# Kernel optimization log

Measured on AMD Instinct MI355X. Metric: run time of the kernel, lower is better.

## Reference

```python
import jax, jax.numpy as jnp
import numpy as np

B, D = 32, 2048


def setup_inputs() -> dict:
    key = jax.random.key(0)
    ks = jax.random.split(key, 7)
    # torch init: weights ~ N(0, 0.1^2); biases default Linear uniform(-1/sqrt(D), 1/sqrt(D))
    bound = 1.0 / np.sqrt(D)
    return {
        "x": jax.random.normal(ks[0], (B, D), dtype=jnp.float32),
        "Wq": 0.1 * jax.random.normal(ks[1], (D, D), dtype=jnp.float32),
        "bq": jax.random.uniform(ks[2], (D,), minval=-bound, maxval=bound, dtype=jnp.float32),
        "Wk": 0.1 * jax.random.normal(ks[3], (D, D), dtype=jnp.float32),
        "bk": jax.random.uniform(ks[4], (D,), minval=-bound, maxval=bound, dtype=jnp.float32),
        "Wv": 0.1 * jax.random.normal(ks[5], (D, D), dtype=jnp.float32),
        "bv": jax.random.uniform(ks[6], (D,), minval=-bound, maxval=bound, dtype=jnp.float32),
    }


def reference(x, Wq, bq, Wk, bk, Wv, bv):
    # q,k,v: [B, D] feature-wise projections (torch Linear: x @ W^T + b)
    q = x @ Wq.T + bq
    k = x @ Wk.T + bk
    v = x @ Wv.T + bv
    # rank-1 outer product scores[b,i,j] = q[b,i] * k[b,j]  -> [B, D, D]
    scores = q[:, :, None] * k[:, None, :]
    # softmax over dim=1 (as in the original F.softmax(..., dim=1))
    weights = jax.nn.softmax(scores, axis=1)
    # weighted V sum: out[b,i] = sum_j weights[b,i,j] * v[b,j]  -> [B, D]
    out = jnp.einsum("bij,bj->bi", weights, v)
    return out
```

## Files before the change

kernel.cpp:

```cpp
#include <hip/hip_runtime.h>
#include <math.h>


#define D 2048
#define BATCH 32
#define SEG 132
#define NPART 8

#define PART_STRIDE 196608
#define KDP_OFF 1572864
#define NP_OFF  1708032

#define L2E 1.4426950408889634f

typedef short s16x8 __attribute__((ext_vector_type(8)));
typedef float f32x4 __attribute__((ext_vector_type(4)));

union FragU { s16x8 v; unsigned u[4]; };

__device__ __forceinline__ float fast_exp2(float x) {
#if __has_builtin(__builtin_amdgcn_exp2f)
  return __builtin_amdgcn_exp2f(x);
#else
  return exp2f(x);
#endif
}
__device__ __forceinline__ unsigned pack_rne(float a, float b) {
  unsigned ua = __float_as_uint(a), ub = __float_as_uint(b);
  ua = ua + 0x7FFFu + ((ua >> 16) & 1u);
  ub = ub + 0x7FFFu + ((ub >> 16) & 1u);
  return (ua >> 16) | (ub & 0xFFFF0000u);
}
__device__ __forceinline__ void pack8(const float4& fa, const float4& fb,
                                      FragU& h) {
  h.u[0] = pack_rne(fa.x, fa.y);
  h.u[1] = pack_rne(fa.z, fa.w);
  h.u[2] = pack_rne(fb.x, fb.y);
  h.u[3] = pack_rne(fb.z, fb.w);
}
__device__ __forceinline__ float sum_parts(const float* __restrict__ ws,
                                           size_t o) {
  float s0 = ws[o] + ws[o + PART_STRIDE];
  float s1 = ws[o + 2 * PART_STRIDE] + ws[o + 3 * PART_STRIDE];
  float s2 = ws[o + 4 * PART_STRIDE] + ws[o + 5 * PART_STRIDE];
  float s3 = ws[o + 6 * PART_STRIDE] + ws[o + 7 * PART_STRIDE];
  return (s0 + s1) + (s2 + s3);
}

__global__ __launch_bounds__(256, 4) void k1_proj(
    const float* __restrict__ x, const float* __restrict__ Wq,
    const float* __restrict__ Wk, const float* __restrict__ Wv,
    float* __restrict__ ws) {
  __shared__ float red[4][512];
  const int tid = threadIdx.x;
  const int lane = tid & 63, wv = tid >> 6;
  const int tile = blockIdx.x >> 3, ke = blockIdx.x & 7;
  const int m = tile >> 7, lr = (tile & 127) * 16;
  const float* W = (m == 0) ? Wq : (m == 1) ? Wk : Wv;

  const int kbase = ke * 256 + wv * 64 + (lane >> 4) * 8;
  const float* ap = W + (size_t)(lr + (lane & 15)) * D + kbase;
  const float* xp0 = x + (size_t)(lane & 15) * D + kbase;
  const float* xp1 = xp0 + 16 * D;

  f32x4 acc0 = {0.f, 0.f, 0.f, 0.f}, acc1 = {0.f, 0.f, 0.f, 0.f};
#pragma unroll
  for (int s = 0; s < 2; ++s) {
    const int off = s * 32;
    float4 fa = *(const float4*)(ap + off);
    float4 fb = *(const float4*)(ap + off + 4);
    float4 x0a = *(const float4*)(xp0 + off);
    float4 x0b = *(const float4*)(xp0 + off + 4);
    float4 x1a = *(const float4*)(xp1 + off);
    float4 x1b = *(const float4*)(xp1 + off + 4);
    FragU Ah, Bh0, Bh1;
    pack8(fa, fb, Ah);
    pack8(x0a, x0b, Bh0);
    pack8(x1a, x1b, Bh1);
    acc0 = __builtin_amdgcn_mfma_f32_16x16x32_bf16(Ah.v, Bh0.v, acc0, 0, 0, 0);
    acc1 = __builtin_amdgcn_mfma_f32_16x16x32_bf16(Ah.v, Bh1.v, acc1, 0, 0, 0);
  }
  const int col = lane & 15, rq = (lane >> 4) * 4;
#pragma unroll
  for (int r = 0; r < 4; ++r) {
    red[wv][col * 16 + rq + r] = acc0[r];
    red[wv][(col + 16) * 16 + rq + r] = acc1[r];
  }
  __syncthreads();
  float* part = ws + (size_t)ke * PART_STRIDE + (size_t)m * 65536;
#pragma unroll
  for (int i = tid; i < 512; i += 256) {
    float s = (red[0][i] + red[1][i]) + (red[2][i] + red[3][i]);
    part[(size_t)(i >> 4) * D + lr + (i & 15)] = s;
  }
}

__global__ __launch_bounds__(512, 4) void k3_dz(float* __restrict__ ws,
                                                const float* __restrict__ bq,
                                                const float* __restrict__ bk,
                                                const float* __restrict__ bv) {
  __shared__ float qs[2048];
  __shared__ float zs[512];
  __shared__ float rmx[8], rmn[8];
  __shared__ int cnt[2];
  const int bx = blockIdx.x, t = threadIdx.x;
  const int b = bx >> 4, jc = bx & 15;
  if (t == 0) { cnt[0] = 0; cnt[1] = 0; }

  const size_t qb = (size_t)b * D;
  float4 bb = ((const float4*)bq)[t];
  float4 qv = bb;
#pragma unroll
  for (int p = 0; p < NPART; ++p) {
    float4 pp = ((const float4*)(ws + (size_t)p * PART_STRIDE + qb))[t];
    qv.x += pp.x; qv.y += pp.y; qv.z += pp.z; qv.w += pp.w;
  }
  *(float4*)&qs[t * 4] = qv;
  float mx = fmaxf(fmaxf(qv.x, qv.y), fmaxf(qv.z, qv.w));
  float mn = fminf(fminf(qv.x, qv.y), fminf(qv.z, qv.w));
#pragma unroll
  for (int off = 32; off; off >>= 1) {
    mx = fmaxf(mx, __shfl_down(mx, off));
    mn = fminf(mn, __shfl_down(mn, off));
  }
  if ((t & 63) == 0) { rmx[t >> 6] = mx; rmn[t >> 6] = mn; }
  __syncthreads();
  mx = rmx[0]; mn = rmn[0];
#pragma unroll
  for (int w = 1; w < 8; ++w) {
    mx = fmaxf(mx, rmx[w]);
    mn = fminf(mn, rmn[w]);
  }

  const int jl = t & 127, ih = t >> 7;
  const int j = jc * 128 + jl;
  const float k2 = (sum_parts(ws, 65536 + qb + j) + bk[j]) * L2E;
  const float m2 = (k2 >= 0.f) ? k2 * mx : k2 * mn;
  const float nm2 = -m2;
  const float* qp = qs + ih * 512;
  float z0 = 0.f, z1 = 0.f, z2 = 0.f, z3 = 0.f;
#pragma unroll 8
  for (int i = 0; i < 512; i += 4) {
    float4 q4 = *(const float4*)&qp[i];
    z0 += fast_exp2(fmaf(q4.x, k2, nm2));
    z1 += fast_exp2(fmaf(q4.y, k2, nm2));
    z2 += fast_exp2(fmaf(q4.z, k2, nm2));
    z3 += fast_exp2(fmaf(q4.w, k2, nm2));
  }
  zs[t] = (z0 + z1) + (z2 + z3);
  __syncthreads();

  float2* kdp = (float2*)(ws + KDP_OFF) + ((size_t)b * 16 + jc) * SEG;
  if (t < 128) {
    float Z = (zs[t] + zs[t + 128]) + (zs[t + 256] + zs[t + 384]);
    float v = sum_parts(ws, 131072 + qb + j) + bv[j];
    float d = __log2f(fabsf(v) / Z) - m2;
    int slot;
    if (v >= 0.f) slot = atomicAdd(&cnt[0], 1);
    else          slot = (SEG - 1) - atomicAdd(&cnt[1], 1);
    kdp[slot] = make_float2(k2, d);
  }
  __syncthreads();
  const int npos = cnt[0];
  if (t < 4) kdp[npos + t] = make_float2(0.f, -1e30f);
  if (t == 0) ((int*)(ws + NP_OFF))[b * 16 + jc] = npos;
}

__global__ __launch_bounds__(512, 4) void k4_out(const float* __restrict__ ws,
                                                 const float* __restrict__ bq,
                                                 float* __restrict__ out) {
  __shared__ float2 kd[16 * SEG];
  __shared__ int np[16];
  __shared__ float rs[512];
  const int bx = blockIdx.x, t = threadIdx.x;
  const int b = bx >> 4, ic = bx & 15;

  const float4* src = (const float4*)((const float2*)(ws + KDP_OFF) +
                                      (size_t)b * 16 * SEG);
  for (int idx = t; idx < (16 * SEG) / 2; idx += 512)
    ((float4*)kd)[idx] = src[idx];
  if (t < 16) np[t] = ((const int*)(ws + NP_OFF))[b * 16 + t];

  const int il = t & 127, jh = t >> 7;
  const int i = ic * 128 + il;
  const size_t io = (size_t)b * D + i;
  const float qi = sum_parts(ws, io) + bq[i];
  __syncthreads();

  float p0 = 0.f, p1 = 0.f, p2 = 0.f, p3 = 0.f;
  float n0 = 0.f, n1 = 0.f, n2 = 0.f, n3 = 0.f;
#pragma unroll
  for (int s = jh * 4; s < jh * 4 + 4; ++s) {
    const float2* seg = kd + s * SEG;
    const int npos = np[s];
    const int pe = (npos + 3) & ~3;
    const int ns = (npos + 4) & ~3;
    for (int jj = 0; jj < pe; jj += 4) {
      float4 t0 = *(const float4*)&seg[jj];
      float4 t1 = *(const float4*)&seg[jj + 2];
      p0 += fast_exp2(fmaf(qi, t0.x, t0.y));
      p1 += fast_exp2(fmaf(qi, t0.z, t0.w));
      p2 += fast_exp2(fmaf(qi, t1.x, t1.y));
      p3 += fast_exp2(fmaf(qi, t1.z, t1.w));
    }
    for (int jj = ns; jj < SEG; jj += 4) {
      float4 t0 = *(const float4*)&seg[jj];
      float4 t1 = *(const float4*)&seg[jj + 2];
      n0 += fast_exp2(fmaf(qi, t0.x, t0.y));
      n1 += fast_exp2(fmaf(qi, t0.z, t0.w));
      n2 += fast_exp2(fmaf(qi, t1.x, t1.y));
      n3 += fast_exp2(fmaf(qi, t1.z, t1.w));
    }
  }
  rs[t] = ((p0 + p1) + (p2 + p3)) - ((n0 + n1) + (n2 + n3));
  __syncthreads();
  if (t < 128)
    out[io] = (rs[il] + rs[il + 128]) + (rs[il + 256] + rs[il + 384]);
}

extern "C" void kernel_launch(void* const* d_in, const int* in_sizes, int n_in,
                              void* d_out, int out_size, void* d_ws, size_t ws_size,
                              hipStream_t stream) {
  (void)in_sizes; (void)n_in; (void)out_size; (void)ws_size;
  const float* x  = (const float*)d_in[0];
  const float* Wq = (const float*)d_in[1];
  const float* bq = (const float*)d_in[2];
  const float* Wk = (const float*)d_in[3];
  const float* bk = (const float*)d_in[4];
  const float* Wv = (const float*)d_in[5];
  const float* bv = (const float*)d_in[6];
  float* ws  = (float*)d_ws;
  float* out = (float*)d_out;

  k1_proj<<<3072, 256, 0, stream>>>(x, Wq, Wk, Wv, ws);
  k3_dz<<<512, 512, 0, stream>>>(ws, bq, bk, bv);
  k4_out<<<512, 512, 0, stream>>>(ws, bq, out);
}
```

Baseline: 144.3 us.

## Halve K-split partials in projection, double block count in softmax kernels

The projection kernel now splits K into 4 parts instead of 8, so each block does 4 MFMA steps with all loads hoisted ahead. This halves the partial-sum buffers written to the workspace and later reduced. The dz and output kernels now use 64-column chunks across 1024 blocks, with smaller per-chunk segments (SEGF=68) and 8-way in-block reductions, to raise parallelism and occupancy. The trade-off is more register pressure in the projection kernel, which also drops to a launch bound of 2, and twice as many blocks redundantly recomputing q and its max/min in the dz kernel.

```diff
diff --git a/kernel.cpp b/kernel.cpp
--- a/kernel.cpp
+++ b/kernel.cpp
@@ -4,12 +4,12 @@
 
 #define D 2048
 #define BATCH 32
-#define SEG 132
-#define NPART 8
+#define SEGF 68
+#define NPART 4
 
 #define PART_STRIDE 196608
-#define KDP_OFF 1572864
-#define NP_OFF  1708032
+#define KDP_OFF 786432
+#define NP_OFF  925696
 
 #define L2E 1.4426950408889634f
 
@@ -42,41 +42,44 @@
                                            size_t o) {
   float s0 = ws[o] + ws[o + PART_STRIDE];
   float s1 = ws[o + 2 * PART_STRIDE] + ws[o + 3 * PART_STRIDE];
-  float s2 = ws[o + 4 * PART_STRIDE] + ws[o + 5 * PART_STRIDE];
-  float s3 = ws[o + 6 * PART_STRIDE] + ws[o + 7 * PART_STRIDE];
-  return (s0 + s1) + (s2 + s3);
-}
-
-__global__ __launch_bounds__(256, 4) void k1_proj(
+  return s0 + s1;
+}
+
+__global__ __launch_bounds__(256, 2) void k1_proj(
     const float* __restrict__ x, const float* __restrict__ Wq,
     const float* __restrict__ Wk, const float* __restrict__ Wv,
     float* __restrict__ ws) {
   __shared__ float red[4][512];
   const int tid = threadIdx.x;
   const int lane = tid & 63, wv = tid >> 6;
-  const int tile = blockIdx.x >> 3, ke = blockIdx.x & 7;
+  const int tile = blockIdx.x >> 2, kq = blockIdx.x & 3;
   const int m = tile >> 7, lr = (tile & 127) * 16;
   const float* W = (m == 0) ? Wq : (m == 1) ? Wk : Wv;
 
-  const int kbase = ke * 256 + wv * 64 + (lane >> 4) * 8;
+  const int kbase = kq * 512 + wv * 128 + (lane >> 4) * 8;
   const float* ap = W + (size_t)(lr + (lane & 15)) * D + kbase;
   const float* xp0 = x + (size_t)(lane & 15) * D + kbase;
   const float* xp1 = xp0 + 16 * D;
 
+  float4 fa[4], fb[4], x0a[4], x0b[4], x1a[4], x1b[4];
+#pragma unroll
+  for (int s = 0; s < 4; ++s) {
+    const int off = s * 32;
+    fa[s] = *(const float4*)(ap + off);
+    fb[s] = *(const float4*)(ap + off + 4);
+    x0a[s] = *(const float4*)(xp0 + off);
+    x0b[s] = *(const float4*)(xp0 + off + 4);
+    x1a[s] = *(const float4*)(xp1 + off);
+    x1b[s] = *(const float4*)(xp1 + off + 4);
+  }
+
   f32x4 acc0 = {0.f, 0.f, 0.f, 0.f}, acc1 = {0.f, 0.f, 0.f, 0.f};
 #pragma unroll
-  for (int s = 0; s < 2; ++s) {
-    const int off = s * 32;
-    float4 fa = *(const float4*)(ap + off);
-    float4 fb = *(const float4*)(ap + off + 4);
-    float4 x0a = *(const float4*)(xp0 + off);
-    float4 x0b = *(const float4*)(xp0 + off + 4);
-    float4 x1a = *(const float4*)(xp1 + off);
-    float4 x1b = *(const float4*)(xp1 + off + 4);
+  for (int s = 0; s < 4; ++s) {
     FragU Ah, Bh0, Bh1;
-    pack8(fa, fb, Ah);
-    pack8(x0a, x0b, Bh0);
-    pack8(x1a, x1b, Bh1);
+    pack8(fa[s], fb[s], Ah);
+    pack8(x0a[s], x0b[s], Bh0);
+    pack8(x1a[s], x1b[s], Bh1);
     acc0 = __builtin_amdgcn_mfma_f32_16x16x32_bf16(Ah.v, Bh0.v, acc0, 0, 0, 0);
     acc1 = __builtin_amdgcn_mfma_f32_16x16x32_bf16(Ah.v, Bh1.v, acc1, 0, 0, 0);
   }
@@ -87,7 +90,7 @@
     red[wv][(col + 16) * 16 + rq + r] = acc1[r];
   }
   __syncthreads();
-  float* part = ws + (size_t)ke * PART_STRIDE + (size_t)m * 65536;
+  float* part = ws + (size_t)kq * PART_STRIDE + (size_t)m * 65536;
 #pragma unroll
   for (int i = tid; i < 512; i += 256) {
     float s = (red[0][i] + red[1][i]) + (red[2][i] + red[3][i]);
@@ -95,7 +98,7 @@
   }
 }
 
-__global__ __launch_bounds__(512, 4) void k3_dz(float* __restrict__ ws,
+__global__ __launch_bounds__(512, 8) void k3_dz(float* __restrict__ ws,
                                                 const float* __restrict__ bq,
                                                 const float* __restrict__ bk,
                                                 const float* __restrict__ bv) {
@@ -104,17 +107,19 @@
   __shared__ float rmx[8], rmn[8];
   __shared__ int cnt[2];
   const int bx = blockIdx.x, t = threadIdx.x;
-  const int b = bx >> 4, jc = bx & 15;
+  const int b = bx >> 5, jc = bx & 31;
   if (t == 0) { cnt[0] = 0; cnt[1] = 0; }
 
   const size_t qb = (size_t)b * D;
+  float4 p0 = ((const float4*)(ws + qb))[t];
+  float4 p1 = ((const float4*)(ws + PART_STRIDE + qb))[t];
+  float4 p2 = ((const float4*)(ws + 2 * PART_STRIDE + qb))[t];
+  float4 p3 = ((const float4*)(ws + 3 * PART_STRIDE + qb))[t];
   float4 bb = ((const float4*)bq)[t];
-  float4 qv = bb;
-#pragma unroll
-  for (int p = 0; p < NPART; ++p) {
-    float4 pp = ((const float4*)(ws + (size_t)p * PART_STRIDE + qb))[t];
-    qv.x += pp.x; qv.y += pp.y; qv.z += pp.z; qv.w += pp.w;
-  }
+  float4 qv = {(p0.x + p1.x) + (p2.x + p3.x) + bb.x,
+               (p0.y + p1.y) + (p2.y + p3.y) + bb.y,
+               (p0.z + p1.z) + (p2.z + p3.z) + bb.z,
+               (p0.w + p1.w) + (p2.w + p3.w) + bb.w};
   *(float4*)&qs[t * 4] = qv;
   float mx = fmaxf(fmaxf(qv.x, qv.y), fmaxf(qv.z, qv.w));
   float mn = fminf(fminf(qv.x, qv.y), fminf(qv.z, qv.w));
@@ -132,15 +137,15 @@
     mn = fminf(mn, rmn[w]);
   }
 
-  const int jl = t & 127, ih = t >> 7;
-  const int j = jc * 128 + jl;
+  const int jl = t & 63, ih = t >> 6;
+  const int j = jc * 64 + jl;
   const float k2 = (sum_parts(ws, 65536 + qb + j) + bk[j]) * L2E;
   const float m2 = (k2 >= 0.f) ? k2 * mx : k2 * mn;
   const float nm2 = -m2;
-  const float* qp = qs + ih * 512;
+  const float* qp = qs + ih * 256;
   float z0 = 0.f, z1 = 0.f, z2 = 0.f, z3 = 0.f;
 #pragma unroll 8
-  for (int i = 0; i < 512; i += 4) {
+  for (int i = 0; i < 256; i += 4) {
     float4 q4 = *(const float4*)&qp[i];
     z0 += fast_exp2(fmaf(q4.x, k2, nm2));
     z1 += fast_exp2(fmaf(q4.y, k2, nm2));
@@ -150,39 +155,40 @@
   zs[t] = (z0 + z1) + (z2 + z3);
   __syncthreads();
 
-  float2* kdp = (float2*)(ws + KDP_OFF) + ((size_t)b * 16 + jc) * SEG;
-  if (t < 128) {
-    float Z = (zs[t] + zs[t + 128]) + (zs[t + 256] + zs[t + 384]);
+  float2* kdp = (float2*)(ws + KDP_OFF) + ((size_t)b * 32 + jc) * SEGF;
+  if (t < 64) {
+    float Z = ((zs[t] + zs[t + 64]) + (zs[t + 128] + zs[t + 192])) +
+              ((zs[t + 256] + zs[t + 320]) + (zs[t + 384] + zs[t + 448]));
     float v = sum_parts(ws, 131072 + qb + j) + bv[j];
     float d = __log2f(fabsf(v) / Z) - m2;
     int slot;
     if (v >= 0.f) slot = atomicAdd(&cnt[0], 1);
-    else          slot = (SEG - 1) - atomicAdd(&cnt[1], 1);
+    else          slot = (SEGF - 1) - atomicAdd(&cnt[1], 1);
     kdp[slot] = make_float2(k2, d);
   }
   __syncthreads();
   const int npos = cnt[0];
   if (t < 4) kdp[npos + t] = make_float2(0.f, -1e30f);
-  if (t == 0) ((int*)(ws + NP_OFF))[b * 16 + jc] = npos;
-}
-
-__global__ __launch_bounds__(512, 4) void k4_out(const float* __restrict__ ws,
+  if (t == 0) ((int*)(ws + NP_OFF))[b * 32 + jc] = npos;
+}
+
+__global__ __launch_bounds__(512, 8) void k4_out(const float* __restrict__ ws,
                                                  const float* __restrict__ bq,
                                                  float* __restrict__ out) {
-  __shared__ float2 kd[16 * SEG];
-  __shared__ int np[16];
+  __shared__ float2 kd[32 * SEGF];
+  __shared__ int np[32];
   __shared__ float rs[512];
   const int bx = blockIdx.x, t = threadIdx.x;
-  const int b = bx >> 4, ic = bx & 15;
+  const int b = bx >> 5, ic = bx & 31;
 
   const float4* src = (const float4*)((const float2*)(ws + KDP_OFF) +
-                                      (size_t)b * 16 * SEG);
-  for (int idx = t; idx < (16 * SEG) / 2; idx += 512)
+                                      (size_t)b * 32 * SEGF);
+  for (int idx = t; idx < (32 * SEGF) / 2; idx += 512)
     ((float4*)kd)[idx] = src[idx];
-  if (t < 16) np[t] = ((const int*)(ws + NP_OFF))[b * 16 + t];
-
-  const int il = t & 127, jh = t >> 7;
-  const int i = ic * 128 + il;
+  if (t < 32) np[t] = ((const int*)(ws + NP_OFF))[b * 32 + t];
+
+  const int il = t & 63, jh = t >> 6;
+  const int i = ic * 64 + il;
   const size_t io = (size_t)b * D + i;
   const float qi = sum_parts(ws, io) + bq[i];
   __syncthreads();
@@ -191,7 +197,7 @@
   float n0 = 0.f, n1 = 0.f, n2 = 0.f, n3 = 0.f;
 #pragma unroll
   for (int s = jh * 4; s < jh * 4 + 4; ++s) {
-    const float2* seg = kd + s * SEG;
+    const float2* seg = kd + s * SEGF;
     const int npos = np[s];
     const int pe = (npos + 3) & ~3;
     const int ns = (npos + 4) & ~3;
@@ -203,7 +209,7 @@
       p2 += fast_exp2(fmaf(qi, t1.x, t1.y));
       p3 += fast_exp2(fmaf(qi, t1.z, t1.w));
     }
-    for (int jj = ns; jj < SEG; jj += 4) {
+    for (int jj = ns; jj < SEGF; jj += 4) {
       float4 t0 = *(const float4*)&seg[jj];
       float4 t1 = *(const float4*)&seg[jj + 2];
       n0 += fast_exp2(fmaf(qi, t0.x, t0.y));
@@ -214,8 +220,9 @@
   }
   rs[t] = ((p0 + p1) + (p2 + p3)) - ((n0 + n1) + (n2 + n3));
   __syncthreads();
-  if (t < 128)
-    out[io] = (rs[il] + rs[il + 128]) + (rs[il + 256] + rs[il + 384]);
+  if (t < 64)
+    out[io] = ((rs[il] + rs[il + 64]) + (rs[il + 128] + rs[il + 192])) +
+              ((rs[il + 256] + rs[il + 320]) + (rs[il + 384] + rs[il + 448]));
 }
 
 extern "C" void kernel_launch(void* const* d_in, const int* in_sizes, int n_in,
@@ -232,7 +239,7 @@
   float* ws  = (float*)d_ws;
   float* out = (float*)d_out;
 
-  k1_proj<<<3072, 256, 0, stream>>>(x, Wq, Wk, Wv, ws);
-  k3_dz<<<512, 512, 0, stream>>>(ws, bq, bk, bv);
-  k4_out<<<512, 512, 0, stream>>>(ws, bq, out);
-}
+  k1_proj<<<1536, 256, 0, stream>>>(x, Wq, Wk, Wv, ws);
+  k3_dz<<<1024, 512, 0, stream>>>(ws, bq, bk, bv);
+  k4_out<<<1024, 512, 0, stream>>>(ws, bq, out);
+}
```

Measured after the change: 141.7 us. Within noise of the previous version (-1.8%).
